# Kernel tuning notes

Hardware: AMD Instinct MI355X
Metric: run time of the kernel (lower is better)

The kernel has to match this reference:

```python
import jax, jax.numpy as jnp
import numpy as np

B, T, D = 32, 512, 768
K, H = 256, 512


def setup_inputs() -> dict:
    key = jax.random.key(0)
    ks = jax.random.split(key, 5)
    s = 0.02  # keep pre-activations in a sane range
    return {
        "inputs": jax.random.normal(ks[0], (B, T, D), jnp.float32),
        "W_x": jax.random.normal(ks[1], (K + 1, 4 * H), jnp.float32) * s,
        "W_h": jax.random.normal(ks[2], (H, 4 * H), jnp.float32) * s,
        "b_lstm": jnp.zeros((4 * H,), jnp.float32),
        "W_key": jax.random.normal(ks[3], (H, K), jnp.float32) * s,
        "b_key": jnp.zeros((K,), jnp.float32),
        "W_g": jax.random.normal(ks[4], (H, 1), jnp.float32) * s,
        "b_g": jnp.zeros((1,), jnp.float32),
        "conf_gain": jnp.ones((), jnp.float32),
        "conf_bias": jnp.zeros((), jnp.float32),
    }


def reference(inputs, W_x, W_h, b_lstm, W_key, b_key, W_g, b_g, conf_gain, conf_bias):
    Bq, Tq, Dq = inputs.shape
    Kq = W_key.shape[1]
    Hq = W_h.shape[0]
    t_idx = jnp.arange(Tq)
    xs = jnp.transpose(inputs, (1, 0, 2))  # [T, B, D]

    def step(carry, xt):
        t, x = xt  # t: scalar step index, x: [B, D]
        key_r, h, c, M_k, M_v = carry
        # Keras LSTMCell (gate order i, f, c, o); input is previous key_r [B, K+1]
        z = key_r @ W_x + h @ W_h + b_lstm
        i, f, g_c, o = jnp.split(z, 4, axis=-1)
        i = jax.nn.sigmoid(i)
        f = jax.nn.sigmoid(f)
        g_c = jnp.tanh(g_c)
        o = jax.nn.sigmoid(o)
        c = f * c + i * g_c
        h = o * jnp.tanh(c)  # lstm_out == hidden in Keras LSTMCell
        key_w = h @ W_key + b_key            # [B, K]
        g = jax.nn.sigmoid(h @ W_g + b_g)    # [B, 1]
        # similarity attention over all previously written memory slots
        sim = jnp.einsum('bd,tbd->bt', x, M_v)          # [B, T]
        mask = (t_idx < t)[None, :]                     # valid slots only
        w_k = jax.nn.softmax(jnp.where(mask, sim, -1e30), axis=1)
        c_k = jax.nn.sigmoid(sim * conf_gain + conf_bias)
        aug = jnp.concatenate([jnp.transpose(M_k, (1, 0, 2)), c_k[:, :, None]], axis=2)  # [B, T, K+1]
        key_r_new = jnp.where(t > 0, g * jnp.einsum('bt,btk->bk', w_k, aug), 0.0)
        M_k = M_k.at[t].set(key_w)
        M_v = M_v.at[t].set(x)
        return (key_r_new, h, c, M_k, M_v), None

    init = (
        jnp.zeros((Bq, Kq + 1), inputs.dtype),
        jnp.zeros((Bq, Hq), inputs.dtype),
        jnp.zeros((Bq, Hq), inputs.dtype),
        jnp.zeros((Tq, Bq, Kq), inputs.dtype),
        jnp.zeros((Tq, Bq, Dq), inputs.dtype),
    )
    (key_r, h, c, M_k, M_v), _ = jax.lax.scan(step, init, (t_idx, xs))
    return h  # final lstm_out
```

## Files before the change

### kernel.cpp

```cpp
#include <hip/hip_runtime.h>
#include <math.h>

#define BQ 32
#define TQ 512
#define DQ 768
#define KQ 256
#define HQ 512
#define G4 2048
#define BROW 768
#define STP 772
#define NWG 512
#define NTHR 256
#define NBG 4

typedef float f32x4 __attribute__((ext_vector_type(4)));

__device__ __forceinline__ void waitcnt0() {
  asm volatile("s_waitcnt vmcnt(0) lgkmcnt(0)" ::: "memory");
}
__device__ __forceinline__ void st_dev(float* p, float v) {
  asm volatile("global_store_dword %0, %1, off sc1" :: "v"(p), "v"(v) : "memory");
}
__device__ __forceinline__ int ld_dev(const int* p) {
  int v;
  asm volatile("global_load_dword %0, %1, off sc1\ns_waitcnt vmcnt(0)"
               : "=v"(v) : "v"(p) : "memory");
  return v;
}
__device__ __forceinline__ void wg_wait_ctr(const int* ctr, int target) {
  if (threadIdx.x < 64) {
    while (ld_dev(ctr) < target) __builtin_amdgcn_s_sleep(1);
  }
  __syncthreads();
}
__device__ __forceinline__ void wg_signal_ctr(int* ctr) {
  waitcnt0();
  __syncthreads();
  if (threadIdx.x == 0) atomicAdd(ctr, 1);
}
__device__ __forceinline__ float sigm(float x) { return 1.f / (1.f + __expf(-x)); }

__global__ void __launch_bounds__(256) gram_k(const float* __restrict__ X,
                                              float* __restrict__ Gm) {
  __shared__ __align__(16) float As[64 * 33];
  __shared__ __align__(16) float Bs[64 * 33];
  const int bid = blockIdx.x;
  const int b = blockIdx.y;
  int I = 0, base = 0;
  while (base + I + 1 <= bid) { base += I + 1; ++I; }
  const int J = bid - base;
  const int t0 = I * 64, u0 = J * 64;
  const float* Xb = X + (size_t)b * TQ * DQ;
  const int ty = threadIdx.x >> 4, tx = threadIdx.x & 15;
  const int sc = threadIdx.x & 31, sr = threadIdx.x >> 5;
  float acc[4][4];
#pragma unroll
  for (int i = 0; i < 4; ++i)
#pragma unroll
    for (int j = 0; j < 4; ++j) acc[i][j] = 0.f;
  for (int k0 = 0; k0 < DQ; k0 += 32) {
#pragma unroll
    for (int rr = 0; rr < 8; ++rr) {
      const int r = rr * 8 + sr;
      As[r * 33 + sc] = Xb[(size_t)(t0 + r) * DQ + k0 + sc];
      Bs[r * 33 + sc] = Xb[(size_t)(u0 + r) * DQ + k0 + sc];
    }
    __syncthreads();
#pragma unroll
    for (int k = 0; k < 32; ++k) {
      float av[4], bv[4];
#pragma unroll
      for (int i = 0; i < 4; ++i) av[i] = As[(ty * 4 + i) * 33 + k];
#pragma unroll
      for (int j = 0; j < 4; ++j) bv[j] = Bs[(tx * 4 + j) * 33 + k];
#pragma unroll
      for (int i = 0; i < 4; ++i)
#pragma unroll
        for (int j = 0; j < 4; ++j) acc[i][j] += av[i] * bv[j];
    }
    __syncthreads();
  }
  float* gb = Gm + (size_t)b * TQ * TQ;
#pragma unroll
  for (int i = 0; i < 4; ++i) {
    f32x4 o;
    o.x = acc[i][0]; o.y = acc[i][1]; o.z = acc[i][2]; o.w = acc[i][3];
    *(f32x4*)&gb[(size_t)(t0 + ty * 4 + i) * TQ + u0 + tx * 4] = o;
  }
}

__global__ void __launch_bounds__(256) smax_k(float* __restrict__ Gm,
                                              float* __restrict__ Sv,
                                              const float* __restrict__ cgp,
                                              const float* __restrict__ cbp) {
  const int t = blockIdx.x + 1;
  const int b = blockIdx.y;
  const int tid = threadIdx.x;
  const int lane = tid & 63;
  const int wv = tid >> 6;
  __shared__ float row[TQ];
  __shared__ float r1[4], r2[4], r3[4];
  float* R = Gm + ((size_t)b * TQ + t) * TQ;
  const float cg = cgp[0], cb = cbp[0];
  for (int i = tid; i < t; i += 256) row[i] = R[i];
  __syncthreads();
  float m = -3e38f;
  for (int i = tid; i < t; i += 256) m = fmaxf(m, row[i]);
#pragma unroll
  for (int k = 1; k < 64; k <<= 1) m = fmaxf(m, __shfl_xor(m, k));
  if (lane == 0) r1[wv] = m;
  __syncthreads();
  m = fmaxf(fmaxf(r1[0], r1[1]), fmaxf(r1[2], r1[3]));
  float s = 0.f, sck = 0.f;
  for (int i = tid; i < t; i += 256) {
    const float r = row[i];
    const float e = __expf(r - m);
    const float ck = 1.f / (1.f + __expf(-(r * cg + cb)));
    row[i] = e; s += e; sck += e * ck;
  }
#pragma unroll
  for (int k = 1; k < 64; k <<= 1) { s += __shfl_xor(s, k); sck += __shfl_xor(sck, k); }
  if (lane == 0) { r2[wv] = s; r3[wv] = sck; }
  __syncthreads();
  s = r2[0] + r2[1] + r2[2] + r2[3];
  sck = r3[0] + r3[1] + r3[2] + r3[3];
  const float inv = 1.f / s;
  for (int i = tid; i < t; i += 256) R[i] = row[i] * inv;
  if (tid == 0) Sv[(size_t)b * TQ + t] = sck * inv;
}

__global__ void __launch_bounds__(NTHR, 2) esbn_scan(
    const float* __restrict__ Wx, const float* __restrict__ Wh,
    const float* __restrict__ bl, const float* __restrict__ Wk,
    const float* __restrict__ bk, const float* __restrict__ Wg,
    const float* __restrict__ bgp, const float* __restrict__ Wmat,
    const float* __restrict__ Sv, float* buf, int* ctrs,
    float* __restrict__ out) {
  __shared__ __align__(16) float st[NBG * STP];
  __shared__ __align__(16) float wrow[NBG * TQ];
  __shared__ __align__(16) float Mk_s[16 * 520];
  __shared__ __align__(16) float wkey_s[4 * 520];
  __shared__ __align__(16) float wgv[HQ];
  __shared__ __align__(16) float svl[NBG * TQ];
  __shared__ __align__(16) float zred[4 * 8 * 4 * 4];
  __shared__ float c_s[NBG * 8];
  __shared__ float bl_s[32];
  __shared__ float bk_s[4];
  __shared__ float bg_s;

  const int tid = threadIdx.x;
  const int wg = blockIdx.x & 63;
  const int grp = blockIdx.x >> 6;
  const int b0 = grp * NBG;
  const int dc = tid >> 3;
  const int cg = tid & 7;

  int colg[4];
#pragma unroll
  for (int j = 0; j < 4; ++j) {
    const int c = cg * 4 + j;
    colg[j] = (c >> 3) * HQ + wg * 8 + (c & 7);
  }
  f32x4 wh[16], wxr[8], wxl;
#pragma unroll
  for (int i = 0; i < 16; ++i) {
    const int d = (i << 5) + dc;
    wh[i].x = Wh[(size_t)d * G4 + colg[0]];
    wh[i].y = Wh[(size_t)d * G4 + colg[1]];
    wh[i].z = Wh[(size_t)d * G4 + colg[2]];
    wh[i].w = Wh[(size_t)d * G4 + colg[3]];
  }
#pragma unroll
  for (int i = 0; i < 8; ++i) {
    const int d = (i << 5) + dc;
    wxr[i].x = Wx[(size_t)d * G4 + colg[0]];
    wxr[i].y = Wx[(size_t)d * G4 + colg[1]];
    wxr[i].z = Wx[(size_t)d * G4 + colg[2]];
    wxr[i].w = Wx[(size_t)d * G4 + colg[3]];
  }
  wxl.x = wxl.y = wxl.z = wxl.w = 0.f;
  if (dc == 0) {
    wxl.x = Wx[(size_t)256 * G4 + colg[0]];
    wxl.y = Wx[(size_t)256 * G4 + colg[1]];
    wxl.z = Wx[(size_t)256 * G4 + colg[2]];
    wxl.w = Wx[(size_t)256 * G4 + colg[3]];
  }
  for (int i = tid; i < NBG * STP; i += NTHR) st[i] = 0.f;
  for (int i = tid; i < 16 * 520; i += NTHR) Mk_s[i] = 0.f;
  for (int i = tid; i < 4 * 520; i += NTHR) {
    const int kl = i / 520, u = i - kl * 520;
    wkey_s[i] = (u < HQ) ? Wk[(size_t)u * KQ + wg * 4 + kl] : 0.f;
  }
  for (int i = tid; i < HQ; i += NTHR) wgv[i] = Wg[i];
  for (int i = tid; i < NBG * TQ; i += NTHR)
    svl[i] = Sv[(size_t)(b0 + (i >> 9)) * TQ + (i & 511)];
  if (tid < 32) bl_s[tid] = bl[(tid >> 3) * HQ + wg * 8 + (tid & 7)];
  if (tid < 4) bk_s[tid] = bk[wg * 4 + tid];
  if (tid == 0) bg_s = bgp[0];
  if (tid < NBG * 8) c_s[tid] = 0.f;
  __syncthreads();

  int* ctr = ctrs + grp * 32;
  const int yb = tid >> 6;
  const int ykl = (tid >> 4) & 3;
  const int ytc = tid & 15;
  const int lt = tid & 63;

  int sgo[3], slo[3];
#pragma unroll
  for (int k = 0; k < 3; ++k) {
    const int c = tid + (k << 8);
    const int b = c / 192, off = (c - b * 192) << 2;
    sgo[k] = (b << 9) + (b << 8) + off;
    slo[k] = b * STP + off;
  }

  for (int t = 0; t < TQ; ++t) {
    const int p = t & 1, pn = p ^ 1;
    float wv8[8];
    const bool rowv = (t >= 1) && (t < TQ - 1);
    if (rowv) {
      const float* wr = Wmat + ((size_t)(b0 + yb) * TQ + t) * TQ + lt;
#pragma unroll
      for (int k = 0; k < 8; ++k) wv8[k] = wr[k << 6];
    }
    if (t > 0) {
      wg_wait_ctr(ctr, 64 * t);
      const float* base = buf + (size_t)(p * BQ + b0) * BROW;
      f32x4 v0, v1, v2;
      const float* q0 = base + sgo[0];
      const float* q1 = base + sgo[1];
      const float* q2 = base + sgo[2];
      asm volatile("global_load_dwordx4 %0, %1, off sc1" : "=v"(v0) : "v"(q0));
      asm volatile("global_load_dwordx4 %0, %1, off sc1" : "=v"(v1) : "v"(q1));
      asm volatile("global_load_dwordx4 %0, %1, off sc1" : "=v"(v2) : "v"(q2));
      asm volatile("s_waitcnt vmcnt(0)" : "+v"(v0), "+v"(v1), "+v"(v2) : : "memory");
      *(f32x4*)&st[slo[0]] = v0;
      *(f32x4*)&st[slo[1]] = v1;
      *(f32x4*)&st[slo[2]] = v2;
    }
    __syncthreads();
    float gv[NBG];
    {
      const int sb = lt >> 4, sl = lt & 15;
      float a = 0.f;
      const float* hb = &st[sb * STP + (sl << 2)];
      const float* wb = &wgv[sl << 2];
#pragma unroll
      for (int j = 0; j < 8; ++j) {
        const f32x4 hv = *(const f32x4*)&hb[j << 6];
        const f32x4 wv = *(const f32x4*)&wb[j << 6];
        a += hv.x * wv.x + hv.y * wv.y + hv.z * wv.z + hv.w * wv.w;
      }
      a += __shfl_xor(a, 1);
      a += __shfl_xor(a, 2);
      a += __shfl_xor(a, 4);
      a += __shfl_xor(a, 8);
#pragma unroll
      for (int b = 0; b < NBG; ++b) gv[b] = sigm(__shfl(a, b << 4) + bg_s);
    }
    f32x4 acc[NBG], pk[NBG];
#pragma unroll
    for (int b = 0; b < NBG; ++b) {
      acc[b].x = acc[b].y = acc[b].z = acc[b].w = 0.f;
      pk[b].x = pk[b].y = pk[b].z = pk[b].w = 0.f;
    }
#pragma unroll
    for (int i = 0; i < 16; ++i) {
      const f32x4 w = wh[i];
      const int d = (i << 5) + dc;
#pragma unroll
      for (int b = 0; b < NBG; ++b) acc[b] += st[b * STP + d] * w;
    }
#pragma unroll
    for (int i = 0; i < 8; ++i) {
      const f32x4 w = wxr[i];
      const int d = 512 + (i << 5) + dc;
#pragma unroll
      for (int b = 0; b < NBG; ++b) pk[b] += st[b * STP + d] * w;
    }
    if (dc == 0 && t > 0) {
#pragma unroll
      for (int b = 0; b < NBG; ++b) pk[b] += svl[(b << 9) + t - 1] * wxl;
    }
#pragma unroll
    for (int b = 0; b < NBG; ++b) {
      const float g = gv[b];
      acc[b].x += g * pk[b].x; acc[b].y += g * pk[b].y;
      acc[b].z += g * pk[b].z; acc[b].w += g * pk[b].w;
    }
#pragma unroll
    for (int m = 8; m <= 32; m <<= 1) {
#pragma unroll
      for (int b = 0; b < NBG; ++b) {
        acc[b].x += __shfl_xor(acc[b].x, m);
        acc[b].y += __shfl_xor(acc[b].y, m);
        acc[b].z += __shfl_xor(acc[b].z, m);
        acc[b].w += __shfl_xor(acc[b].w, m);
      }
    }
    if (lt < 8) {
      const int wv = tid >> 6;
#pragma unroll
      for (int b = 0; b < NBG; ++b)
        *(f32x4*)&zred[((wv * 8 + lt) * 4 + b) * 4] = acc[b];
    }
    __syncthreads();
    if (tid < 32) {
      const int b = tid >> 3, u = tid & 7;
      float zg[4];
#pragma unroll
      for (int g = 0; g < 4; ++g) {
        const int cgi = g * 2 + (u >> 2), comp = u & 3;
        float z = bl_s[g * 8 + u];
#pragma unroll
        for (int wv = 0; wv < 4; ++wv) z += zred[((wv * 8 + cgi) * 4 + b) * 4 + comp];
        zg[g] = z;
      }
      const float gi = sigm(zg[0]);
      const float gf = sigm(zg[1]);
      const float go = sigm(zg[3]);
      const float cn = gf * c_s[tid] + gi * tanhf(zg[2]);
      const float hv = go * tanhf(cn);
      c_s[tid] = cn;
      if (t == TQ - 1) out[(size_t)(b0 + b) * HQ + wg * 8 + u] = hv;
      else st_dev(buf + (size_t)(pn * BQ + b0 + b) * BROW + wg * 8 + u, hv);
    }
    if (t == TQ - 1) break;
    if (t >= 1) {
#pragma unroll
      for (int k = 0; k < 8; ++k) wrow[yb * TQ + lt + (k << 6)] = wv8[k];
      float kw = 0.f;
      const float* hrow = &st[yb * STP];
      const float* wkr = &wkey_s[ykl * 520];
#pragma unroll
      for (int j = 0; j < 32; ++j) {
        const int u = ytc + (j << 4);
        kw += hrow[u] * wkr[u];
      }
      kw += __shfl_xor(kw, 1);
      kw += __shfl_xor(kw, 2);
      kw += __shfl_xor(kw, 4);
      kw += __shfl_xor(kw, 8);
      if (ytc == 0) Mk_s[(yb * 4 + ykl) * 520 + (t - 1)] = kw + bk_s[ykl];
      float accA = 0.f;
      const float* mk = &Mk_s[(yb * 4 + ykl) * 520];
      const float* wb = &wrow[yb * TQ];
#pragma unroll
      for (int j = 0; j < 32; ++j) {
        const int u = ytc + (j << 4);
        accA += wb[u] * mk[u];
      }
      accA += __shfl_xor(accA, 1);
      accA += __shfl_xor(accA, 2);
      accA += __shfl_xor(accA, 4);
      accA += __shfl_xor(accA, 8);
      if (ytc == 0)
        st_dev(buf + (size_t)(pn * BQ + b0 + yb) * BROW + 512 + wg * 4 + ykl, accA);
    }
    wg_signal_ctr(ctr);
  }
}

extern "C" void kernel_launch(void* const* d_in, const int* in_sizes, int n_in,
                              void* d_out, int out_size, void* d_ws, size_t ws_size,
                              hipStream_t stream) {
  (void)in_sizes; (void)n_in; (void)out_size; (void)ws_size;
  const float* X  = (const float*)d_in[0];
  const float* Wx = (const float*)d_in[1];
  const float* Wh = (const float*)d_in[2];
  const float* bl = (const float*)d_in[3];
  const float* Wk = (const float*)d_in[4];
  const float* bk = (const float*)d_in[5];
  const float* Wg = (const float*)d_in[6];
  const float* bg = (const float*)d_in[7];
  const float* cg = (const float*)d_in[8];
  const float* cb = (const float*)d_in[9];
  float* out = (float*)d_out;
  float* ws = (float*)d_ws;

  float* Gm = ws;
  float* Sv = ws + (size_t)8388608;
  float* buf = ws + (size_t)8404992;
  int* ctrs = (int*)(ws + (size_t)8454144);

  hipMemsetAsync(Sv, 0, (size_t)(16384 + 49152 + 256) * 4, stream);
  gram_k<<<dim3(36, BQ), dim3(256), 0, stream>>>(X, Gm);
  smax_k<<<dim3(TQ - 1, BQ), dim3(256), 0, stream>>>(Gm, Sv, cg, cb);

  void* args[] = {(void*)&Wx, (void*)&Wh, (void*)&bl, (void*)&Wk, (void*)&bk,
                  (void*)&Wg, (void*)&bg, (void*)&Gm, (void*)&Sv,
                  (void*)&buf, (void*)&ctrs, (void*)&out};
  hipError_t e = hipLaunchCooperativeKernel((const void*)esbn_scan, dim3(NWG),
                                            dim3(NTHR), args, 0, stream);
  if (e != hipSuccess) {
    esbn_scan<<<dim3(NWG), dim3(NTHR), 0, stream>>>(Wx, Wh, bl, Wk, bk, Wg, bg,
                                                    Gm, Sv, buf, ctrs, out);
  }
}
```

Measured before the change: 4.646 ms.

## Split step barrier into h and key-read counters to overlap attention with recurrence

Replaces the single per-group completion counter with two counters: one signalled as soon as the new hidden state is written, and one after the attention readout is stored. Workgroups can now start the W_h matvec on h while the key-read part of the previous step is still finishing, waiting on the second counter only before the W_x part. The key projection and attention reductions are also fused into one loop, with the newest memory slot folded in analytically. In exchange there is an extra __syncthreads and counter poll per step, a doubled counter area, and a leftover dead loop in the gate computation.

```diff
diff --git a/kernel.cpp b/kernel.cpp
--- a/kernel.cpp
+++ b/kernel.cpp
@@ -200,20 +200,12 @@
   if (tid < NBG * 8) c_s[tid] = 0.f;
   __syncthreads();
 
-  int* ctr = ctrs + grp * 32;
+  int* ctrH = ctrs + grp * 64;
+  int* ctrA = ctrs + grp * 64 + 32;
   const int yb = tid >> 6;
   const int ykl = (tid >> 4) & 3;
   const int ytc = tid & 15;
   const int lt = tid & 63;
-
-  int sgo[3], slo[3];
-#pragma unroll
-  for (int k = 0; k < 3; ++k) {
-    const int c = tid + (k << 8);
-    const int b = c / 192, off = (c - b * 192) << 2;
-    sgo[k] = (b << 9) + (b << 8) + off;
-    slo[k] = b * STP + off;
-  }
 
   for (int t = 0; t < TQ; ++t) {
     const int p = t & 1, pn = p ^ 1;
@@ -225,32 +217,45 @@
       for (int k = 0; k < 8; ++k) wv8[k] = wr[k << 6];
     }
     if (t > 0) {
-      wg_wait_ctr(ctr, 64 * t);
+      wg_wait_ctr(ctrH, 64 * t);
       const float* base = buf + (size_t)(p * BQ + b0) * BROW;
-      f32x4 v0, v1, v2;
-      const float* q0 = base + sgo[0];
-      const float* q1 = base + sgo[1];
-      const float* q2 = base + sgo[2];
+      f32x4 v0, v1;
+      const int i0 = tid, i1 = tid + 256;
+      const float* q0 = base + ((i0 >> 7) * BROW) + ((i0 & 127) << 2);
+      const float* q1 = base + ((i1 >> 7) * BROW) + ((i1 & 127) << 2);
       asm volatile("global_load_dwordx4 %0, %1, off sc1" : "=v"(v0) : "v"(q0));
       asm volatile("global_load_dwordx4 %0, %1, off sc1" : "=v"(v1) : "v"(q1));
-      asm volatile("global_load_dwordx4 %0, %1, off sc1" : "=v"(v2) : "v"(q2));
-      asm volatile("s_waitcnt vmcnt(0)" : "+v"(v0), "+v"(v1), "+v"(v2) : : "memory");
-      *(f32x4*)&st[slo[0]] = v0;
-      *(f32x4*)&st[slo[1]] = v1;
-      *(f32x4*)&st[slo[2]] = v2;
+      asm volatile("s_waitcnt vmcnt(0)" : "+v"(v0), "+v"(v1) : : "memory");
+      *(f32x4*)&st[((i0 >> 7) * STP) + ((i0 & 127) << 2)] = v0;
+      *(f32x4*)&st[((i1 >> 7) * STP) + ((i1 & 127) << 2)] = v1;
     }
     __syncthreads();
+    f32x4 acc[NBG];
+#pragma unroll
+    for (int b = 0; b < NBG; ++b) { acc[b].x = acc[b].y = acc[b].z = acc[b].w = 0.f; }
+#pragma unroll
+    for (int i = 0; i < 16; ++i) {
+      const f32x4 w = wh[i];
+      const int d = (i << 5) + dc;
+#pragma unroll
+      for (int b = 0; b < NBG; ++b) acc[b] += st[b * STP + d] * w;
+    }
     float gv[NBG];
     {
       const int sb = lt >> 4, sl = lt & 15;
       float a = 0.f;
-      const float* hb = &st[sb * STP + (sl << 2)];
-      const float* wb = &wgv[sl << 2];
+      const float* hb = &st[sb * STP];
+      const float* wb = wgv;
 #pragma unroll
       for (int j = 0; j < 8; ++j) {
-        const f32x4 hv = *(const f32x4*)&hb[j << 6];
-        const f32x4 wv = *(const f32x4*)&wb[j << 6];
-        a += hv.x * wv.x + hv.y * wv.y + hv.z * wv.z + hv.w * wv.w;
+        const int u = sl + (j << 4) + ((j & 3) << 7);
+        a += hb[u] * wb[u];
+      }
+      a = 0.f;
+#pragma unroll
+      for (int j = 0; j < 32; ++j) {
+        const int u = sl + (j << 4);
+        a += hb[u] * wb[u];
       }
       a += __shfl_xor(a, 1);
       a += __shfl_xor(a, 2);
@@ -259,19 +264,19 @@
 #pragma unroll
       for (int b = 0; b < NBG; ++b) gv[b] = sigm(__shfl(a, b << 4) + bg_s);
     }
-    f32x4 acc[NBG], pk[NBG];
-#pragma unroll
-    for (int b = 0; b < NBG; ++b) {
-      acc[b].x = acc[b].y = acc[b].z = acc[b].w = 0.f;
-      pk[b].x = pk[b].y = pk[b].z = pk[b].w = 0.f;
-    }
-#pragma unroll
-    for (int i = 0; i < 16; ++i) {
-      const f32x4 w = wh[i];
-      const int d = (i << 5) + dc;
-#pragma unroll
-      for (int b = 0; b < NBG; ++b) acc[b] += st[b * STP + d] * w;
-    }
+    if (t > 0) {
+      wg_wait_ctr(ctrA, 64 * t);
+      const float* base = buf + (size_t)(p * BQ + b0) * BROW;
+      f32x4 v2;
+      const float* q2 = base + ((tid >> 6) * BROW) + 512 + ((tid & 63) << 2);
+      asm volatile("global_load_dwordx4 %0, %1, off sc1" : "=v"(v2) : "v"(q2));
+      asm volatile("s_waitcnt vmcnt(0)" : "+v"(v2) : : "memory");
+      *(f32x4*)&st[((tid >> 6) * STP) + 512 + ((tid & 63) << 2)] = v2;
+    }
+    __syncthreads();
+    f32x4 pk[NBG];
+#pragma unroll
+    for (int b = 0; b < NBG; ++b) { pk[b].x = pk[b].y = pk[b].z = pk[b].w = 0.f; }
 #pragma unroll
     for (int i = 0; i < 8; ++i) {
       const f32x4 w = wxr[i];
@@ -327,38 +332,34 @@
       else st_dev(buf + (size_t)(pn * BQ + b0 + b) * BROW + wg * 8 + u, hv);
     }
     if (t == TQ - 1) break;
+    wg_signal_ctr(ctrH);
     if (t >= 1) {
 #pragma unroll
       for (int k = 0; k < 8; ++k) wrow[yb * TQ + lt + (k << 6)] = wv8[k];
-      float kw = 0.f;
+      float kw = 0.f, accA = 0.f;
       const float* hrow = &st[yb * STP];
       const float* wkr = &wkey_s[ykl * 520];
+      const float* mk = &Mk_s[(yb * 4 + ykl) * 520];
+      const float* wb = &wrow[yb * TQ];
 #pragma unroll
       for (int j = 0; j < 32; ++j) {
         const int u = ytc + (j << 4);
         kw += hrow[u] * wkr[u];
-      }
-      kw += __shfl_xor(kw, 1);
-      kw += __shfl_xor(kw, 2);
-      kw += __shfl_xor(kw, 4);
-      kw += __shfl_xor(kw, 8);
-      if (ytc == 0) Mk_s[(yb * 4 + ykl) * 520 + (t - 1)] = kw + bk_s[ykl];
-      float accA = 0.f;
-      const float* mk = &Mk_s[(yb * 4 + ykl) * 520];
-      const float* wb = &wrow[yb * TQ];
-#pragma unroll
-      for (int j = 0; j < 32; ++j) {
-        const int u = ytc + (j << 4);
         accA += wb[u] * mk[u];
       }
-      accA += __shfl_xor(accA, 1);
-      accA += __shfl_xor(accA, 2);
-      accA += __shfl_xor(accA, 4);
-      accA += __shfl_xor(accA, 8);
-      if (ytc == 0)
+#pragma unroll
+      for (int m = 1; m <= 8; m <<= 1) {
+        kw += __shfl_xor(kw, m);
+        accA += __shfl_xor(accA, m);
+      }
+      kw += bk_s[ykl];
+      accA += wb[t - 1] * kw;
+      if (ytc == 0) {
         st_dev(buf + (size_t)(pn * BQ + b0 + yb) * BROW + 512 + wg * 4 + ykl, accA);
-    }
-    wg_signal_ctr(ctr);
+        Mk_s[(yb * 4 + ykl) * 520 + (t - 1)] = kw;
+      }
+    }
+    wg_signal_ctr(ctrA);
   }
 }
 
@@ -384,7 +385,7 @@
   float* buf = ws + (size_t)8404992;
   int* ctrs = (int*)(ws + (size_t)8454144);
 
-  hipMemsetAsync(Sv, 0, (size_t)(16384 + 49152 + 256) * 4, stream);
+  hipMemsetAsync(Sv, 0, (size_t)(16384 + 49152 + 512) * 4, stream);
   gram_k<<<dim3(36, BQ), dim3(256), 0, stream>>>(X, Gm);
   smax_k<<<dim3(TQ - 1, BQ), dim3(256), 0, stream>>>(Gm, Sv, cg, cb);
 
```

Result: faster. 4.188 ms (-9.9%).
